# Kernel optimization log

Hardware: AMD Instinct MI355X
Metric: run time of the kernel (lower is better)

Reference implementation:

```python
import jax, jax.numpy as jnp
import numpy as np

B, T, V, E, H = 4, 2048, 50257, 1024, 16
D = E // H  # head dim = 64

def _ln(x, g, b, eps=1e-5):
    mu = jnp.mean(x, axis=-1, keepdims=True)
    var = jnp.var(x, axis=-1, keepdims=True)
    return (x - mu) * jax.lax.rsqrt(var + eps) * g + b

def setup_inputs() -> dict:
    key = jax.random.key(0)
    ks = jax.random.split(key, 20)
    s = 0.02
    return {
        "ids": jax.random.randint(ks[0], (B, T), 0, V),
        "wte": jax.random.normal(ks[1], (V, E), jnp.float32) * s,
        "wpe": jax.random.normal(ks[2], (T, E), jnp.float32) * s,
        "wq": jax.random.normal(ks[3], (H, E, D), jnp.float32) * s,
        "wk": jax.random.normal(ks[4], (H, E, D), jnp.float32) * s,
        "wv": jax.random.normal(ks[5], (H, E, D), jnp.float32) * s,
        "bq": jnp.zeros((H, D), jnp.float32),
        "bk": jnp.zeros((H, D), jnp.float32),
        "bv": jnp.zeros((H, D), jnp.float32),
        "wproj": jax.random.normal(ks[6], (E, E), jnp.float32) * s,
        "bproj": jnp.zeros((E,), jnp.float32),
        "ln1_g": jnp.ones((E,), jnp.float32),
        "ln1_b": jnp.zeros((E,), jnp.float32),
        "ln2_g": jnp.ones((E,), jnp.float32),
        "ln2_b": jnp.zeros((E,), jnp.float32),
        "w_fc": jax.random.normal(ks[7], (E, 4 * E), jnp.float32) * s,
        "b_fc": jnp.zeros((4 * E,), jnp.float32),
        "w_out": jax.random.normal(ks[8], (4 * E, E), jnp.float32) * s,
        "b_out": jnp.zeros((E,), jnp.float32),
    }

def reference(ids, wte, wpe, wq, wk, wv, bq, bk, bv, wproj, bproj,
              ln1_g, ln1_b, ln2_g, ln2_b, w_fc, b_fc, w_out, b_out):
    t = ids.shape[1]
    x = wte[ids] + wpe[:t]                      # [B,T,E]
    # --- attention (all heads batched; faithful per-head math) ---
    h = _ln(x, ln1_g, ln1_b)
    q = jnp.einsum('btc,hcd->bhtd', h, wq) + bq[None, :, None, :]
    k = jnp.einsum('btc,hcd->bhtd', h, wk) + bk[None, :, None, :]
    v = jnp.einsum('btc,hcd->bhtd', h, wv) + bv[None, :, None, :]
    scores = jnp.einsum('bhtd,bhsd->bhts', q, k) * (1.0 / np.sqrt(D))
    causal = jnp.tril(jnp.ones((t, t), bool))
    scores = jnp.where(causal, scores, -jnp.inf)
    attn = jax.nn.softmax(scores, axis=-1)      # dropout = identity (eval)
    o = jnp.einsum('bhts,bhsd->bhtd', attn, v)
    o = jnp.transpose(o, (0, 2, 1, 3)).reshape(x.shape[0], t, E)  # concat heads
    x = x + o @ wproj + bproj
    # --- MLP ---
    h2 = _ln(x, ln2_g, ln2_b)
    m = jax.nn.gelu(h2 @ w_fc + b_fc, approximate=False) @ w_out + b_out
    return x + m
```

## Files before the change

### kernel.cpp

```cpp
#include <hip/hip_runtime.h>
#include <math.h>

#define BB 4
#define TT 2048
#define EE 1024
#define HH 16
#define DD 64
#define MM (BB*TT)

typedef unsigned short u16;
typedef __bf16 bf16x8 __attribute__((ext_vector_type(8)));
typedef float  f32x4  __attribute__((ext_vector_type(4)));

__device__ inline float bf2f(u16 u){ union{unsigned int i; float f;} v; v.i=((unsigned int)u)<<16; return v.f; }
__device__ inline u16 f2bf(float f){ union{float f; unsigned int i;} v; v.f=f; return (u16)((v.i + 0x7fffu + ((v.i>>16)&1u))>>16); }
__device__ inline u16 f2bf_trunc(float f){ union{float f; unsigned int i;} v; v.f=f; return (u16)(v.i>>16); }

__device__ inline void gload_lds16(const void* g, void* l){
  __builtin_amdgcn_global_load_lds((__attribute__((address_space(1))) void*)g,
                                   (__attribute__((address_space(3))) void*)l, 16, 0, 0);
}

__global__ __launch_bounds__(256) void transpose_tile(
    const float* __restrict__ W, u16* __restrict__ WT, int N, int K)
{
    __shared__ float t[32][33];
    const int n0 = blockIdx.x*32, k0 = blockIdx.y*32;
    const int tx = threadIdx.x, ty = threadIdx.y;
    #pragma unroll
    for (int j=0;j<4;j++)
        t[ty + j*8][tx] = W[(size_t)(k0 + ty + j*8)*N + n0 + tx];
    __syncthreads();
    #pragma unroll
    for (int j=0;j<4;j++)
        WT[(size_t)(n0 + ty + j*8)*K + k0 + tx] = f2bf(t[tx][ty + j*8]);
}

__global__ __launch_bounds__(256) void transpose_v(
    const u16* __restrict__ V, u16* __restrict__ VT)
{
    __shared__ u16 t[32][34];
    const int bh = blockIdx.z;
    const int t0 = blockIdx.x*32;
    const int d0 = blockIdx.y*32;
    const int tx = threadIdx.x, ty = threadIdx.y;
    const u16* Vb = V + (size_t)bh*TT*DD;
    u16* VTb = VT + (size_t)bh*TT*DD;
    #pragma unroll
    for (int j=0;j<4;j++)
        t[ty+j*8][tx] = Vb[(size_t)(t0+ty+j*8)*DD + d0+tx];
    __syncthreads();
    #pragma unroll
    for (int j=0;j<4;j++)
        VTb[(size_t)(d0+ty+j*8)*TT + t0+tx] = t[tx][ty+j*8];
}

__global__ __launch_bounds__(256) void repack_qkv_tiled(
    const float* __restrict__ wq, const float* __restrict__ wk, const float* __restrict__ wv,
    u16* __restrict__ WT)
{
    __shared__ float t[32][33];
    const int z = blockIdx.z, which = z>>4, hh = z&15;
    const int d0 = blockIdx.x*32, c0 = blockIdx.y*32;
    const int tx = threadIdx.x, ty = threadIdx.y;
    const float* w = which==0 ? wq : (which==1 ? wk : wv);
    #pragma unroll
    for (int j=0;j<4;j++)
        t[ty + j*8][tx] = w[((size_t)hh*EE + c0 + ty + j*8)*DD + d0 + tx];
    __syncthreads();
    #pragma unroll
    for (int j=0;j<4;j++)
        WT[(size_t)(which*1024 + hh*64 + d0 + ty + j*8)*1024 + c0 + tx] = f2bf(t[tx][ty + j*8]);
}

__global__ __launch_bounds__(256) void copy_bias_qkv(
    const float* __restrict__ bq, const float* __restrict__ bk, const float* __restrict__ bv,
    float* __restrict__ bias)
{
    int i = blockIdx.x*256 + threadIdx.x;
    const float* b = i<1024 ? bq : (i<2048 ? bk : bv);
    bias[i] = b[i & 1023];
}

__global__ __launch_bounds__(256) void embed_ln1(
    const int* __restrict__ ids, const float* __restrict__ wte, const float* __restrict__ wpe,
    const float* __restrict__ g, const float* __restrict__ b,
    float* __restrict__ x_out, u16* __restrict__ h_out)
{
    const int token = blockIdx.x;
    const int t = token & (TT-1);
    const int id = ids[token];
    const int tid = threadIdx.x;
    float vals[4]; float s=0.f, s2=0.f;
    #pragma unroll
    for (int i=0;i<4;i++){
        int e = tid + i*256;
        float v = wte[(size_t)id*EE + e] + wpe[(size_t)t*EE + e];
        vals[i]=v; s+=v; s2+=v*v;
    }
    for (int off=32; off>=1; off>>=1){ s += __shfl_xor(s,off); s2 += __shfl_xor(s2,off); }
    __shared__ float red[8];
    int wave=tid>>6, lane=tid&63;
    if (lane==0){ red[wave]=s; red[4+wave]=s2; }
    __syncthreads();
    s = red[0]+red[1]+red[2]+red[3];
    s2 = red[4]+red[5]+red[6]+red[7];
    float mu = s*(1.f/EE);
    float var = s2*(1.f/EE) - mu*mu;
    float rstd = rsqrtf(var + 1e-5f);
    #pragma unroll
    for (int i=0;i<4;i++){
        int e = tid + i*256; float v = vals[i];
        x_out[(size_t)token*EE + e] = v;
        h_out[(size_t)token*EE + e] = f2bf((v-mu)*rstd*g[e] + b[e]);
    }
}

__global__ __launch_bounds__(256) void ln_fwd(
    const float* __restrict__ xin, const float* __restrict__ g, const float* __restrict__ b,
    u16* __restrict__ hout)
{
    const int token = blockIdx.x;
    const int tid = threadIdx.x;
    float vals[4]; float s=0.f, s2=0.f;
    #pragma unroll
    for (int i=0;i<4;i++){
        int e = tid + i*256;
        float v = xin[(size_t)token*EE + e];
        vals[i]=v; s+=v; s2+=v*v;
    }
    for (int off=32; off>=1; off>>=1){ s += __shfl_xor(s,off); s2 += __shfl_xor(s2,off); }
    __shared__ float red[8];
    int wave=tid>>6, lane=tid&63;
    if (lane==0){ red[wave]=s; red[4+wave]=s2; }
    __syncthreads();
    s = red[0]+red[1]+red[2]+red[3];
    s2 = red[4]+red[5]+red[6]+red[7];
    float mu = s*(1.f/EE);
    float var = s2*(1.f/EE) - mu*mu;
    float rstd = rsqrtf(var + 1e-5f);
    #pragma unroll
    for (int i=0;i<4;i++){
        int e = tid + i*256; float v = vals[i];
        hout[(size_t)token*EE + e] = f2bf((v-mu)*rstd*g[e] + b[e]);
    }
}

template<int MODE>
__global__ __launch_bounds__(256) void gemm_bt(
    const u16* __restrict__ A, const u16* __restrict__ BT, const float* __restrict__ bias,
    float* CoutF, const float* resid, u16* __restrict__ CoutH,
    u16* __restrict__ q_out, u16* __restrict__ k_out, u16* __restrict__ v_out,
    int Ndim, int Kdim)
{
    __shared__ u16 As[128*32];
    __shared__ u16 Bs[128*32];
    const int tid = threadIdx.x, wave = tid>>6, lane = tid&63;
    const int quad = lane>>4, l16 = lane&15;
    const int m0 = blockIdx.x<<7, n0 = blockIdx.y<<7;
    const int wm = (wave>>1)<<6, wn = (wave&1)<<6;
    const f32x4 zf = {0.f,0.f,0.f,0.f};
    f32x4 acc[4][4];
    #pragma unroll
    for (int i=0;i<4;i++)
        #pragma unroll
        for (int j=0;j<4;j++) acc[i][j]=zf;

    const int rA = lane>>2;
    const int kA = (lane&3)*8;
    for (int k0=0; k0<Kdim; k0+=32){
        __syncthreads();
        #pragma unroll
        for (int i=0;i<2;i++){
            const int inst = wave*2+i;
            const int row  = inst*16 + rA;
            gload_lds16(A  + (size_t)(m0+row)*Kdim + k0 + kA, &As[inst*512]);
            gload_lds16(BT + (size_t)(n0+row)*Kdim + k0 + kA, &Bs[inst*512]);
        }
        __syncthreads();
        bf16x8 af[4], bfr[4];
        #pragma unroll
        for (int mt=0;mt<4;mt++) af[mt]  = *(const bf16x8*)&As[(wm + mt*16 + l16)*32 + quad*8];
        #pragma unroll
        for (int nt=0;nt<4;nt++) bfr[nt] = *(const bf16x8*)&Bs[(wn + nt*16 + l16)*32 + quad*8];
        #pragma unroll
        for (int mt=0;mt<4;mt++)
            #pragma unroll
            for (int nt=0;nt<4;nt++)
                acc[mt][nt] = __builtin_amdgcn_mfma_f32_16x16x32_bf16(af[mt], bfr[nt], acc[mt][nt], 0, 0, 0);
    }
    #pragma unroll
    for (int mt=0;mt<4;mt++){
        #pragma unroll
        for (int nt=0;nt<4;nt++){
            #pragma unroll
            for (int r=0;r<4;r++){
                int m = m0 + wm + mt*16 + quad*4 + r;
                int n = n0 + wn + nt*16 + l16;
                float v = acc[mt][nt][r] + bias[n];
                if (MODE==0){
                    int which = n>>10, hd = n&1023, hh = hd>>6, d = hd&63;
                    u16* dst = which==0 ? q_out : (which==1 ? k_out : v_out);
                    int bb = m>>11, t = m&(TT-1);
                    dst[(((size_t)(bb*HH+hh)*TT + t)<<6) + d] = f2bf(v);
                } else if (MODE==1){
                    size_t idx = (size_t)m*Ndim + n;
                    CoutF[idx] = resid[idx] + v;
                } else {
                    size_t idx = (size_t)m*Ndim + n;
                    CoutH[idx] = f2bf(0.5f*v*(1.0f + erff(v*0.70710678118f)));
                }
            }
        }
    }
}

__device__ __forceinline__ void attn_proc_tile(
    int kt, int q0, int quad, int l16,
    const u16* Ks, const u16* Vs, u16* Psw,
    const bf16x8 (&qf)[2][2], f32x4 (&oacc)[2][4], float (&lsum)[2][4])
{
    if (kt > ((q0+31)>>6)) return;
    const f32x4 zf = {0.f,0.f,0.f,0.f};
    f32x4 a[2][4];
    #pragma unroll
    for (int m=0;m<2;m++)
        #pragma unroll
        for (int st=0;st<4;st++) a[m][st]=zf;
    #pragma unroll
    for (int h2=0;h2<2;h2++){
        #pragma unroll
        for (int st=0;st<4;st++){
            const int s = st*16 + l16;
            const int jc = h2*4 + quad;
            bf16x8 kf = *(const bf16x8*)&Ks[s*64 + (jc ^ (s&7))*8];
            #pragma unroll
            for (int m=0;m<2;m++)
                a[m][st] = __builtin_amdgcn_mfma_f32_16x16x32_bf16(qf[m][h2], kf, a[m][st], 0,0,0);
        }
    }
    const bool needMask = (kt*64 + 63 > q0);
    #pragma unroll
    for (int m=0;m<2;m++){
        const int q0m = q0 + m*16;
        #pragma unroll
        for (int st=0;st<4;st++){
            #pragma unroll
            for (int r=0;r<4;r++){
                float p = exp2f(fminf(a[m][st][r]*0.1803369f, 40.f));
                if (needMask){
                    const int qrow = q0m + quad*4 + r;
                    const int s = kt*64 + st*16 + l16;
                    if (s > qrow) p = 0.f;
                }
                lsum[m][r] += p;
                const int ql = m*16 + quad*4 + r;
                const int sc3 = st*2 + (l16>>3);
                Psw[ql*64 + (sc3 ^ (ql&7))*8 + (l16&7)] = f2bf_trunc(p);
            }
        }
    }
    #pragma unroll
    for (int kh=0; kh<2; kh++){
        const int jc = kh*4 + quad;
        bf16x8 pf[2];
        #pragma unroll
        for (int m=0;m<2;m++){
            const int ql16 = m*16 + l16;
            pf[m] = *(const bf16x8*)&Psw[ql16*64 + (jc ^ (ql16&7))*8];
        }
        #pragma unroll
        for (int dt=0; dt<4; dt++){
            const int d = dt*16 + l16;
            bf16x8 vf = *(const bf16x8*)&Vs[d*64 + (jc ^ (d&7))*8];
            #pragma unroll
            for (int m=0;m<2;m++)
                oacc[m][dt] = __builtin_amdgcn_mfma_f32_16x16x32_bf16(pf[m], vf, oacc[m][dt], 0,0,0);
        }
    }
}

__global__ __launch_bounds__(256,2) void attn_kernel(
    const u16* __restrict__ Q, const u16* __restrict__ K, const u16* __restrict__ VT,
    u16* __restrict__ O)
{
    __shared__ u16 Ks[64*64];
    __shared__ u16 Vs[64*64];
    __shared__ u16 Ps[4*2048];
    const int tid = threadIdx.x, wave = tid>>6, lane = tid&63;
    const int quad = lane>>4, l16 = lane&15;
    const int id = blockIdx.x;
    const int bh   = (id&7) | ((id>>6)<<3);
    const int pair = (id>>3)&7;
    const int qtA = pair, qtB = 15-pair;
    const size_t base = (size_t)bh*TT*DD;
    const u16* Qb = Q + base;
    const u16* Kb = K + base;
    const u16* VTb = VT + base;
    const int qA0 = qtA*128 + wave*32;
    const int qB0 = qtB*128 + wave*32;
    u16* Psw = &Ps[wave*2048];

    bf16x8 qfA[2][2], qfB[2][2];
    #pragma unroll
    for (int m=0;m<2;m++)
        #pragma unroll
        for (int h2=0;h2<2;h2++){
            qfA[m][h2] = *(const bf16x8*)&Qb[(size_t)(qA0+m*16+l16)*DD + h2*32 + quad*8];
            qfB[m][h2] = *(const bf16x8*)&Qb[(size_t)(qB0+m*16+l16)*DD + h2*32 + quad*8];
        }

    const f32x4 zf = {0.f,0.f,0.f,0.f};
    f32x4 oaccA[2][4], oaccB[2][4];
    float lsumA[2][4], lsumB[2][4];
    #pragma unroll
    for (int m=0;m<2;m++){
        #pragma unroll
        for (int dt=0;dt<4;dt++){ oaccA[m][dt]=zf; oaccB[m][dt]=zf; }
        #pragma unroll
        for (int r=0;r<4;r++){ lsumA[m][r]=0.f; lsumB[m][r]=0.f; }
    }

    const int ktMax = 31 - 2*pair;

    const int c0 = wave*64 + lane, c1 = 256 + wave*64 + lane;
    const int r0 = c0>>3, j0 = (c0&7) ^ (r0&7);
    const int r1 = c1>>3, j1 = (c1&7) ^ (r1&7);

    for (int kt=0; kt<=ktMax; kt++){
        __syncthreads();
        {
            const int s0 = kt*64;
            gload_lds16(Kb  + (size_t)(s0+r0)*DD + j0*8, &Ks[wave*512]);
            gload_lds16(Kb  + (size_t)(s0+r1)*DD + j1*8, &Ks[(4+wave)*512]);
            gload_lds16(VTb + (size_t)r0*TT + s0 + j0*8, &Vs[wave*512]);
            gload_lds16(VTb + (size_t)r1*TT + s0 + j1*8, &Vs[(4+wave)*512]);
        }
        __syncthreads();
        attn_proc_tile(kt, qB0, quad, l16, Ks, Vs, Psw, qfB, oaccB, lsumB);
        attn_proc_tile(kt, qA0, quad, l16, Ks, Vs, Psw, qfA, oaccA, lsumA);
    }

    #pragma unroll
    for (int off=1; off<16; off<<=1)
        #pragma unroll
        for (int m=0;m<2;m++)
            #pragma unroll
            for (int r=0;r<4;r++){
                lsumA[m][r] += __shfl_xor(lsumA[m][r], off);
                lsumB[m][r] += __shfl_xor(lsumB[m][r], off);
            }

    const int bb = bh>>4, hh = bh&15;
    #pragma unroll
    for (int m=0;m<2;m++)
        #pragma unroll
        for (int dt=0;dt<4;dt++)
            #pragma unroll
            for (int r=0;r<4;r++){
                int t = qA0 + m*16 + quad*4 + r;
                O[(size_t)(bb*TT + t)*EE + hh*64 + dt*16 + l16] = f2bf(oaccA[m][dt][r] / lsumA[m][r]);
                t = qB0 + m*16 + quad*4 + r;
                O[(size_t)(bb*TT + t)*EE + hh*64 + dt*16 + l16] = f2bf(oaccB[m][dt][r] / lsumB[m][r]);
            }
}

extern "C" void kernel_launch(void* const* d_in, const int* in_sizes, int n_in,
                              void* d_out, int out_size, void* d_ws, size_t ws_size,
                              hipStream_t stream)
{
    (void)in_sizes; (void)n_in; (void)out_size; (void)ws_size;
    const int*   ids  = (const int*)d_in[0];
    const float* wte  = (const float*)d_in[1];
    const float* wpe  = (const float*)d_in[2];
    const float* wq   = (const float*)d_in[3];
    const float* wk   = (const float*)d_in[4];
    const float* wv   = (const float*)d_in[5];
    const float* bq   = (const float*)d_in[6];
    const float* bk   = (const float*)d_in[7];
    const float* bv   = (const float*)d_in[8];
    const float* wproj= (const float*)d_in[9];
    const float* bproj= (const float*)d_in[10];
    const float* ln1g = (const float*)d_in[11];
    const float* ln1b = (const float*)d_in[12];
    const float* ln2g = (const float*)d_in[13];
    const float* ln2b = (const float*)d_in[14];
    const float* wfc  = (const float*)d_in[15];
    const float* bfc  = (const float*)d_in[16];
    const float* wout = (const float*)d_in[17];
    const float* bout = (const float*)d_in[18];

    const size_t MTOK = (size_t)MM*EE;
    char* p = (char*)d_ws;
    float* x    = (float*)p;  p += MTOK*sizeof(float);
    u16*  h     = (u16*)p;    p += MTOK*sizeof(u16);
    u16*  Qb    = (u16*)p;    p += MTOK*sizeof(u16);
    u16*  Kb    = (u16*)p;    p += MTOK*sizeof(u16);
    u16*  Vb    = (u16*)p;    p += MTOK*sizeof(u16);
    u16*  Ob    = (u16*)p;    p += MTOK*sizeof(u16);
    u16*  fcact = Qb;
    u16*  VTv   = h;
    u16*  WqkvT = (u16*)p;    p += (size_t)3072*1024*sizeof(u16);
    float* biasq= (float*)p;  p += 3072*sizeof(float);
    u16*  wprojT= (u16*)p;    p += (size_t)1024*1024*sizeof(u16);
    u16*  wfcT  = (u16*)p;    p += (size_t)4096*1024*sizeof(u16);
    u16*  woutT = (u16*)p;    p += (size_t)1024*4096*sizeof(u16);
    float* out  = (float*)d_out;

    repack_qkv_tiled<<<dim3(2,32,48),dim3(32,8),0,stream>>>(wq,wk,wv,WqkvT);
    copy_bias_qkv<<<12,256,0,stream>>>(bq,bk,bv,biasq);
    transpose_tile<<<dim3(32,32), dim3(32,8),0,stream>>>(wproj, wprojT, 1024, 1024);
    transpose_tile<<<dim3(128,32),dim3(32,8),0,stream>>>(wfc,   wfcT,   4096, 1024);
    transpose_tile<<<dim3(32,128),dim3(32,8),0,stream>>>(wout,  woutT,  1024, 4096);
    embed_ln1<<<MM,256,0,stream>>>(ids, wte, wpe, ln1g, ln1b, x, h);
    gemm_bt<0><<<dim3(64,24),256,0,stream>>>(h, WqkvT, biasq, nullptr,nullptr,nullptr, Qb,Kb,Vb, 3072, 1024);
    transpose_v<<<dim3(64,2,64),dim3(32,8),0,stream>>>(Vb, VTv);
    attn_kernel<<<512,256,0,stream>>>(Qb,Kb,VTv,Ob);
    gemm_bt<1><<<dim3(64,8),256,0,stream>>>(Ob, wprojT, bproj, x, x, nullptr, nullptr,nullptr,nullptr, 1024, 1024);
    ln_fwd<<<MM,256,0,stream>>>(x, ln2g, ln2b, h);
    gemm_bt<2><<<dim3(64,32),256,0,stream>>>(h, wfcT, bfc, nullptr,nullptr, fcact, nullptr,nullptr,nullptr, 4096, 1024);
    gemm_bt<1><<<dim3(64,8),256,0,stream>>>(fcact, woutT, bout, out, x, nullptr, nullptr,nullptr,nullptr, 1024, 4096);
}
```

Baseline: 758.1 us.

## Replace GEMM with 256x256 double-buffered swizzled-LDS pipelined kernel

Replaces the 128x128, K=32, single-buffered GEMM with a 256x256 tile, K=64 kernel using 512 threads. It double-buffers LDS with XOR-swizzled layout, interleaves async global-to-LDS loads with MFMA phases under vmcnt waits and raw barriers, raises MFMA priority, and remaps block IDs for XCD locality. The aim is to hide load latency, raise data reuse per tile, and cut barrier and bank-conflict overhead. It uses 128KB of LDS and many accumulator registers, and the small projection GEMMs launch only 128 blocks, which can leave CUs underused.

```diff
diff --git a/kernel.cpp b/kernel.cpp
--- a/kernel.cpp
+++ b/kernel.cpp
@@ -146,57 +146,117 @@
     }
 }
 
+
+#define VMCNT(N) asm volatile("s_waitcnt vmcnt(" #N ")" ::: "memory")
+#define BARX() { __builtin_amdgcn_s_barrier(); __builtin_amdgcn_sched_barrier(0); }
+
+__device__ __forceinline__ bf16x8 fld(const u16* base, int row, int j){
+    return *(const bf16x8*)&base[(row<<6) + ((j ^ (row&7))<<3)];
+}
+
 template<int MODE>
-__global__ __launch_bounds__(256) void gemm_bt(
+__global__ __launch_bounds__(512,2) void gemm256(
     const u16* __restrict__ A, const u16* __restrict__ BT, const float* __restrict__ bias,
     float* CoutF, const float* resid, u16* __restrict__ CoutH,
     u16* __restrict__ q_out, u16* __restrict__ k_out, u16* __restrict__ v_out,
     int Ndim, int Kdim)
 {
-    __shared__ u16 As[128*32];
-    __shared__ u16 Bs[128*32];
+    __shared__ alignas(16) u16 As[2][256*64];
+    __shared__ alignas(16) u16 Bs[2][256*64];
     const int tid = threadIdx.x, wave = tid>>6, lane = tid&63;
-    const int quad = lane>>4, l16 = lane&15;
-    const int m0 = blockIdx.x<<7, n0 = blockIdx.y<<7;
-    const int wm = (wave>>1)<<6, wn = (wave&1)<<6;
+    const int quad = (lane>>4)&3, l16 = lane&15;
+    const int wr = wave>>2, wc = wave&3;
+
+    const int nwg = gridDim.x;
+    const int chunk = nwg>>3;
+    int id = blockIdx.x;
+    id = (id&7)*chunk + (id>>3);
+    const int m0 = (id & 31) << 8;
+    const int n0 = (id >> 5) << 8;
+
+    const int rS = tid>>3;
+    const int jS = (tid&7) ^ (rS&7);
+    const size_t off0   = (size_t)rS*Kdim + (size_t)(jS<<3);
+    const size_t ofs64K = (size_t)64*Kdim;
+    const u16* pA = A  + (size_t)m0*Kdim;
+    const u16* pB = BT + (size_t)n0*Kdim;
+
+#define STAGE(ARR, GP, BUF, H, KT)                                             \
+  { const u16* _g = (GP) + (size_t)((H)*128)*Kdim + (size_t)(KT)*64 + off0;    \
+    gload_lds16(_g,          &ARR[BUF][(H)*8192 + wave*512]);                  \
+    gload_lds16(_g + ofs64K, &ARR[BUF][(H)*8192 + 4096 + wave*512]); }
+
+    STAGE(As, pA, 0, 0, 0);
+    STAGE(Bs, pB, 0, 0, 0);
+    STAGE(Bs, pB, 0, 1, 0);
+    STAGE(As, pA, 0, 1, 0);
+    STAGE(As, pA, 1, 0, 1);
+    STAGE(Bs, pB, 1, 0, 1);
+    STAGE(Bs, pB, 1, 1, 1);
+
+    f32x4 acc[8][4];
     const f32x4 zf = {0.f,0.f,0.f,0.f};
-    f32x4 acc[4][4];
-    #pragma unroll
-    for (int i=0;i<4;i++)
+    #pragma unroll
+    for (int i=0;i<8;i++)
         #pragma unroll
         for (int j=0;j<4;j++) acc[i][j]=zf;
 
-    const int rA = lane>>2;
-    const int kA = (lane&3)*8;
-    for (int k0=0; k0<Kdim; k0+=32){
-        __syncthreads();
-        #pragma unroll
-        for (int i=0;i<2;i++){
-            const int inst = wave*2+i;
-            const int row  = inst*16 + rA;
-            gload_lds16(A  + (size_t)(m0+row)*Kdim + k0 + kA, &As[inst*512]);
-            gload_lds16(BT + (size_t)(n0+row)*Kdim + k0 + kA, &Bs[inst*512]);
-        }
-        __syncthreads();
-        bf16x8 af[4], bfr[4];
-        #pragma unroll
-        for (int mt=0;mt<4;mt++) af[mt]  = *(const bf16x8*)&As[(wm + mt*16 + l16)*32 + quad*8];
-        #pragma unroll
-        for (int nt=0;nt<4;nt++) bfr[nt] = *(const bf16x8*)&Bs[(wn + nt*16 + l16)*32 + quad*8];
-        #pragma unroll
-        for (int mt=0;mt<4;mt++)
-            #pragma unroll
-            for (int nt=0;nt<4;nt++)
-                acc[mt][nt] = __builtin_amdgcn_mfma_f32_16x16x32_bf16(af[mt], bfr[nt], acc[mt][nt], 0, 0, 0);
-    }
-    #pragma unroll
-    for (int mt=0;mt<4;mt++){
-        #pragma unroll
-        for (int nt=0;nt<4;nt++){
+    bf16x8 af[4][2], bfr[4][2];
+
+#define LDA(HROW)                                                              \
+  { _Pragma("unroll") for (int mt=0; mt<4; mt++)                               \
+    { _Pragma("unroll") for (int kh=0; kh<2; kh++)                             \
+        af[mt][kh] = fld(Ab, (HROW) + (wr<<6) + (mt<<4) + l16, kh*4+quad); } }
+#define LDB(HROW, NTB)                                                         \
+  { _Pragma("unroll") for (int nt=0; nt<2; nt++)                               \
+    { _Pragma("unroll") for (int kh=0; kh<2; kh++)                             \
+        bfr[(NTB)+nt][kh] = fld(Bb, (HROW) + (wc<<5) + (nt<<4) + l16, kh*4+quad); } }
+#define MFMA16(MT0, NT0)                                                       \
+  __builtin_amdgcn_s_setprio(1);                                               \
+  { _Pragma("unroll") for (int mt=0; mt<4; mt++)                               \
+    { _Pragma("unroll") for (int nt=0; nt<2; nt++)                             \
+      { _Pragma("unroll") for (int kh=0; kh<2; kh++)                           \
+          acc[(MT0)+mt][(NT0)+nt] = __builtin_amdgcn_mfma_f32_16x16x32_bf16(   \
+              af[mt][kh], bfr[(NT0)+nt][kh], acc[(MT0)+mt][(NT0)+nt], 0,0,0);  \
+      } } }                                                                    \
+  __builtin_amdgcn_s_setprio(0);
+
+    const int NT = Kdim>>6;
+    for (int kt=0; kt<NT; ++kt){
+        const int b = kt&1;
+        const u16* Ab = As[b];
+        const u16* Bb = Bs[b];
+        if (kt+1 < NT) { VMCNT(6); } else { VMCNT(0); }
+        BARX();
+        LDA(0); LDB(0,0);
+        if (kt+1 < NT) STAGE(As, pA, b^1, 1, kt+1);
+        MFMA16(0,0);
+        BARX();
+        LDB(128,2);
+        if (kt+2 < NT) STAGE(As, pA, b, 0, kt+2);
+        MFMA16(0,2);
+        BARX();
+        LDA(128);
+        if (kt+2 < NT) STAGE(Bs, pB, b, 0, kt+2);
+        MFMA16(4,2);
+        BARX();
+        if (kt+2 < NT) STAGE(Bs, pB, b, 1, kt+2);
+        MFMA16(4,0);
+    }
+#undef STAGE
+#undef LDA
+#undef LDB
+#undef MFMA16
+
+    #pragma unroll
+    for (int mt=0; mt<8; mt++){
+        const int mrow = m0 + ((mt<4) ? (wr<<6)+(mt<<4) : 128+(wr<<6)+((mt-4)<<4)) + (quad<<2);
+        #pragma unroll
+        for (int nt=0; nt<4; nt++){
+            const int n = n0 + ((nt<2) ? (wc<<5)+(nt<<4) : 128+(wc<<5)+((nt-2)<<4)) + l16;
             #pragma unroll
             for (int r=0;r<4;r++){
-                int m = m0 + wm + mt*16 + quad*4 + r;
-                int n = n0 + wn + nt*16 + l16;
+                const int m = mrow + r;
                 float v = acc[mt][nt][r] + bias[n];
                 if (MODE==0){
                     int which = n>>10, hd = n&1023, hh = hd>>6, d = hd&63;
@@ -413,11 +473,11 @@
     transpose_tile<<<dim3(128,32),dim3(32,8),0,stream>>>(wfc,   wfcT,   4096, 1024);
     transpose_tile<<<dim3(32,128),dim3(32,8),0,stream>>>(wout,  woutT,  1024, 4096);
     embed_ln1<<<MM,256,0,stream>>>(ids, wte, wpe, ln1g, ln1b, x, h);
-    gemm_bt<0><<<dim3(64,24),256,0,stream>>>(h, WqkvT, biasq, nullptr,nullptr,nullptr, Qb,Kb,Vb, 3072, 1024);
+    gemm256<0><<<32*12,512,0,stream>>>(h, WqkvT, biasq, nullptr,nullptr,nullptr, Qb,Kb,Vb, 3072, 1024);
     transpose_v<<<dim3(64,2,64),dim3(32,8),0,stream>>>(Vb, VTv);
     attn_kernel<<<512,256,0,stream>>>(Qb,Kb,VTv,Ob);
-    gemm_bt<1><<<dim3(64,8),256,0,stream>>>(Ob, wprojT, bproj, x, x, nullptr, nullptr,nullptr,nullptr, 1024, 1024);
+    gemm256<1><<<32*4,512,0,stream>>>(Ob, wprojT, bproj, x, x, nullptr, nullptr,nullptr,nullptr, 1024, 1024);
     ln_fwd<<<MM,256,0,stream>>>(x, ln2g, ln2b, h);
-    gemm_bt<2><<<dim3(64,32),256,0,stream>>>(h, wfcT, bfc, nullptr,nullptr, fcact, nullptr,nullptr,nullptr, 4096, 1024);
-    gemm_bt<1><<<dim3(64,8),256,0,stream>>>(fcact, woutT, bout, out, x, nullptr, nullptr,nullptr,nullptr, 1024, 4096);
-}
+    gemm256<2><<<32*16,512,0,stream>>>(h, wfcT, bfc, nullptr,nullptr, fcact, nullptr,nullptr,nullptr, 4096, 1024);
+    gemm256<1><<<32*4,512,0,stream>>>(fcact, woutT, bout, out, x, nullptr, nullptr,nullptr,nullptr, 1024, 4096);
+}
```

After: 783.5 us. +3.3%, slower.
